# Kernel optimization log

Measured on AMD Instinct MI355X. Metric: run time of the kernel, lower is better.

Reference implementation:

```python
import jax, jax.numpy as jnp
import numpy as np


def setup_inputs() -> dict:
    key = jax.random.key(0)
    k1, k2, k3, k4, k5 = jax.random.split(key, 5)
    M, K, N, E = 16384, 2048, 5632, 8  # total_tokens, d_model, expert ffn dim, num_experts
    a = jax.random.normal(k1, (M, K), jnp.float32) * 0.1          # fp8-valued activations (simulated in f32)
    b = jax.random.normal(k2, (E, N, K), jnp.float32) * 0.05      # column-major expert weights [E, N, K]
    scale_a = jax.random.uniform(k3, (M, 1), jnp.float32, 0.5, 1.5)   # per-token dequant scale
    scale_b = jax.random.uniform(k4, (E, 1), jnp.float32, 0.5, 1.5)   # per-expert dequant scale
    cuts = jnp.sort(jax.random.randint(k5, (E - 1,), 0, M)).astype(jnp.int32)
    seg_indptr = jnp.concatenate([jnp.zeros(1, jnp.int32), cuts, jnp.full((1,), M, jnp.int32)])
    return {"a": a, "b": b, "scale_a": scale_a, "scale_b": scale_b,
            "seg_indptr": seg_indptr, "batch_size": E}


def reference(a, b, scale_a, scale_b, seg_indptr, batch_size):
    # Grouped GEMM: for expert e, rows seg_indptr[e]:seg_indptr[e+1] of `a` are
    # multiplied by b[e]^T (b is column-major [E, N, K]).
    M = a.shape[0]
    E = b.shape[0]
    group_sizes = jnp.diff(seg_indptr).astype(jnp.int32)           # [E]
    out = jax.lax.ragged_dot(a, jnp.swapaxes(b, 1, 2), group_sizes)  # [M, N]
    # fp8 w8a8 dequant: per-token scale_a, per-expert scale_b gathered per token
    eid = jnp.clip(jnp.searchsorted(seg_indptr, jnp.arange(M), side='right') - 1, 0, E - 1)
    return out * scale_a * scale_b[eid]
```

## Files before the change

kernel.cpp:

```cpp
#include <hip/hip_runtime.h>


#define BK 32
#define NKSTEP 64
#define KDIM 2048

typedef __attribute__((ext_vector_type(4))) float f32x4;
typedef __attribute__((ext_vector_type(4))) unsigned int u32x4;
using frag_ab = __attribute__((ext_vector_type(8))) short;
using frag_cd = __attribute__((ext_vector_type(4))) float;

__device__ __forceinline__ unsigned int pack_bf2(float x, float y) {
  unsigned int ux = __float_as_uint(x);
  unsigned int uy = __float_as_uint(y);
  ux += 0x7fffu + ((ux >> 16) & 1u);
  uy += 0x7fffu + ((uy >> 16) & 1u);
  return (ux >> 16) | (uy & 0xffff0000u);
}

__device__ __forceinline__ void gload_lds16(const void* g, void* lds) {
  __builtin_amdgcn_global_load_lds(
      (const __attribute__((address_space(1))) unsigned int*)g,
      (__attribute__((address_space(3))) unsigned int*)lds, 16, 0, 0);
}

__global__ __launch_bounds__(256)
void convert_kernel(const float* __restrict__ A, const float* __restrict__ B,
                    unsigned short* __restrict__ wa, unsigned short* __restrict__ wb) {
  constexpr long long NA = 16384LL * 2048;
  constexpr long long NB = 8LL * 5632 * 2048;
  constexpr long long NA8 = NA / 8;
  constexpr long long NTOT = (NA + NB) / 8;
  for (long long c = (long long)blockIdx.x * 256 + threadIdx.x; c < NTOT;
       c += (long long)gridDim.x * 256) {
    const float* src;
    unsigned short* dst;
    long long off;
    if (c < NA8) { src = A; dst = wa; off = c * 8; }
    else         { src = B; dst = wb; off = (c - NA8) * 8; }
    f32x4 v0 = *(const f32x4*)(src + off);
    f32x4 v1 = *(const f32x4*)(src + off + 4);
    u32x4 o;
    o[0] = pack_bf2(v0[0], v0[1]);
    o[1] = pack_bf2(v0[2], v0[3]);
    o[2] = pack_bf2(v1[0], v1[1]);
    o[3] = pack_bf2(v1[2], v1[3]);
    *(u32x4*)(dst + off) = o;
  }
}

__global__ __launch_bounds__(256, 3)
void ggemm_o(const unsigned short* __restrict__ A,
             const unsigned short* __restrict__ B,
             const float* __restrict__ sa,
             const float* __restrict__ sb,
             const int* __restrict__ seg,
             float* __restrict__ C) {
  constexpr int M = 16384, N = 5632, E = 8;
  constexpr int NTC = N / 128;
  const int nwg = (M / 128) * NTC;

  int bid = blockIdx.x;
  int sid = (bid & 7) * (nwg >> 3) + (bid >> 3);
  int mt = sid / NTC, nt = sid % NTC;
  int m0 = mt * 128, n0 = nt * 128;

  int tid = threadIdx.x, lane = tid & 63, w = tid >> 6;
  int wr = (w >> 1) * 64, wc = (w & 1) * 64;
  int l16 = lane & 15, lhi = lane >> 4;

  __shared__ unsigned short Asm[2][128 * 32];
  __shared__ unsigned short Bsm[2][128 * 32];

  int sr = lane >> 2;
  int scol = (((lane & 3) ^ (sr & 3)) * 8);
  const unsigned short* gA = A + (size_t)(m0 + w * 32 + sr) * KDIM + scol;

  int xA[4], xB[4];
#pragma unroll
  for (int i = 0; i < 4; ++i)
    xA[i] = (wr + i * 16 + l16) * 32 + ((lhi ^ (l16 & 3)) * 8);
#pragma unroll
  for (int j = 0; j < 4; ++j)
    xB[j] = (wc + j * 16 + l16) * 32 + ((lhi ^ (l16 & 3)) * 8);

  for (int e = 0; e < E; ++e) {
    int rlo = max(m0, seg[e]);
    int rhi = min(m0 + 128, seg[e + 1]);
    if (rlo >= rhi) continue;
    const unsigned short* gB =
        B + (size_t)e * N * KDIM + (size_t)(n0 + w * 32 + sr) * KDIM + scol;

    frag_cd acc[4][4];
#pragma unroll
    for (int i = 0; i < 4; ++i)
#pragma unroll
      for (int j = 0; j < 4; ++j) acc[i][j] = (frag_cd){0.f, 0.f, 0.f, 0.f};

    auto stage = [&](int b, int kt) {
#pragma unroll
      for (int i = 0; i < 2; ++i) {
        gload_lds16(gA + (size_t)i * 16 * KDIM + kt * BK,
                    &Asm[b][(w * 32 + i * 16) * 32]);
        gload_lds16(gB + (size_t)i * 16 * KDIM + kt * BK,
                    &Bsm[b][(w * 32 + i * 16) * 32]);
      }
    };
    auto compute = [&](int b) {
      frag_ab af[4], bf[4];
#pragma unroll
      for (int i = 0; i < 4; ++i) af[i] = *(const frag_ab*)(&Asm[b][xA[i]]);
#pragma unroll
      for (int j = 0; j < 4; ++j) bf[j] = *(const frag_ab*)(&Bsm[b][xB[j]]);
#pragma unroll
      for (int i = 0; i < 4; ++i)
#pragma unroll
        for (int j = 0; j < 4; ++j)
          acc[i][j] = __builtin_amdgcn_mfma_f32_16x16x32_bf16(
              af[i], bf[j], acc[i][j], 0, 0, 0);
    };

    stage(0, 0);
    __syncthreads();
    for (int kt = 0; kt < NKSTEP; ++kt) {
      if (kt + 1 < NKSTEP) stage((kt + 1) & 1, kt + 1);
      compute(kt & 1);
      __syncthreads();
    }

    float sbe = sb[e];
#pragma unroll
    for (int i = 0; i < 4; ++i) {
#pragma unroll
      for (int r = 0; r < 4; ++r) {
        int grow = m0 + wr + i * 16 + lhi * 4 + r;
        if (grow >= rlo && grow < rhi) {
          float s = sa[grow] * sbe;
          float* Crow = C + (size_t)grow * N + n0 + wc;
#pragma unroll
          for (int j = 0; j < 4; ++j)
            Crow[j * 16 + l16] = acc[i][j][r] * s;
        }
      }
    }
  }
}

extern "C" void kernel_launch(void* const* d_in, const int* in_sizes, int n_in,
                              void* d_out, int out_size, void* d_ws, size_t ws_size,
                              hipStream_t stream) {
  const float* a = (const float*)d_in[0];
  const float* b = (const float*)d_in[1];
  const float* sa = (const float*)d_in[2];
  const float* sb = (const float*)d_in[3];
  const int* seg = (const int*)d_in[4];
  float* out = (float*)d_out;

  constexpr size_t NA = 16384ULL * 2048;
  unsigned short* wa = (unsigned short*)d_ws;
  unsigned short* wb = wa + NA;

  hipLaunchKernelGGL(convert_kernel, dim3(2048), dim3(256), 0, stream, a, b, wa, wb);
  hipLaunchKernelGGL(ggemm_o, dim3(5632), dim3(256), 0, stream,
                     wa, wb, sa, sb, seg, out);
}
```

Measured before the change: 774.0 us.

## Double K-tile depth to 64 and remap workgroups into XCD-local super-tiles

The GEMM K tile grows from 32 to 64, with a new 8-way XOR swizzle for the wider LDS rows. This halves the number of barriers and stage/compute iterations and gives two MFMA k-substeps per sync. The block-to-tile mapping now keeps each XCD on a contiguous band of 16 M-tiles, walked in 8x11 super-tiles, to improve L2 reuse of A and B. LDS use doubles and the occupancy hint drops from 3 to 2 blocks per CU.

```diff
diff --git a/kernel.cpp b/kernel.cpp
--- a/kernel.cpp
+++ b/kernel.cpp
@@ -1,8 +1,8 @@
 #include <hip/hip_runtime.h>
 
 
-#define BK 32
-#define NKSTEP 64
+#define BK 64
+#define NKSTEP 32
 #define KDIM 2048
 
 typedef __attribute__((ext_vector_type(4))) float f32x4;
@@ -49,47 +49,51 @@
   }
 }
 
-__global__ __launch_bounds__(256, 3)
-void ggemm_o(const unsigned short* __restrict__ A,
+__global__ __launch_bounds__(256, 2)
+void ggemm_s(const unsigned short* __restrict__ A,
              const unsigned short* __restrict__ B,
              const float* __restrict__ sa,
              const float* __restrict__ sb,
              const int* __restrict__ seg,
              float* __restrict__ C) {
   constexpr int M = 16384, N = 5632, E = 8;
-  constexpr int NTC = N / 128;
-  const int nwg = (M / 128) * NTC;
 
   int bid = blockIdx.x;
-  int sid = (bid & 7) * (nwg >> 3) + (bid >> 3);
-  int mt = sid / NTC, nt = sid % NTC;
+  int xcd = bid & 7;
+  int r = bid >> 3;
+  int st = r / 88, p = r % 88;
+  int pm = p & 7, pn = p >> 3;
+  int smt = st >> 2, snt = st & 3;
+  int mt = xcd * 16 + smt * 8 + pm;
+  int nt = snt * 11 + pn;
   int m0 = mt * 128, n0 = nt * 128;
 
   int tid = threadIdx.x, lane = tid & 63, w = tid >> 6;
   int wr = (w >> 1) * 64, wc = (w & 1) * 64;
   int l16 = lane & 15, lhi = lane >> 4;
 
-  __shared__ unsigned short Asm[2][128 * 32];
-  __shared__ unsigned short Bsm[2][128 * 32];
+  __shared__ unsigned short Asm[2][128 * 64];
+  __shared__ unsigned short Bsm[2][128 * 64];
 
-  int sr = lane >> 2;
-  int scol = (((lane & 3) ^ (sr & 3)) * 8);
-  const unsigned short* gA = A + (size_t)(m0 + w * 32 + sr) * KDIM + scol;
+  int srow = lane >> 3;
+  int scol = ((lane & 7) ^ srow) * 8;
+  const unsigned short* gA = A + (size_t)(m0 + w * 32 + srow) * KDIM + scol;
 
-  int xA[4], xB[4];
+  int c7 = l16 & 7;
+  int x0 = (lhi ^ c7) * 8;
+  int x1 = ((4 | lhi) ^ c7) * 8;
+  int offA[4], offB[4];
 #pragma unroll
-  for (int i = 0; i < 4; ++i)
-    xA[i] = (wr + i * 16 + l16) * 32 + ((lhi ^ (l16 & 3)) * 8);
+  for (int i = 0; i < 4; ++i) offA[i] = (wr + i * 16 + l16) * 64;
 #pragma unroll
-  for (int j = 0; j < 4; ++j)
-    xB[j] = (wc + j * 16 + l16) * 32 + ((lhi ^ (l16 & 3)) * 8);
+  for (int j = 0; j < 4; ++j) offB[j] = (wc + j * 16 + l16) * 64;
 
   for (int e = 0; e < E; ++e) {
     int rlo = max(m0, seg[e]);
     int rhi = min(m0 + 128, seg[e + 1]);
     if (rlo >= rhi) continue;
     const unsigned short* gB =
-        B + (size_t)e * N * KDIM + (size_t)(n0 + w * 32 + sr) * KDIM + scol;
+        B + (size_t)e * N * KDIM + (size_t)(n0 + w * 32 + srow) * KDIM + scol;
 
     frag_cd acc[4][4];
 #pragma unroll
@@ -99,25 +103,31 @@
 
     auto stage = [&](int b, int kt) {
 #pragma unroll
-      for (int i = 0; i < 2; ++i) {
-        gload_lds16(gA + (size_t)i * 16 * KDIM + kt * BK,
-                    &Asm[b][(w * 32 + i * 16) * 32]);
-        gload_lds16(gB + (size_t)i * 16 * KDIM + kt * BK,
-                    &Bsm[b][(w * 32 + i * 16) * 32]);
+      for (int i = 0; i < 4; ++i) {
+        gload_lds16(gA + (size_t)i * 8 * KDIM + kt * BK,
+                    &Asm[b][(w * 32 + i * 8) * 64]);
+        gload_lds16(gB + (size_t)i * 8 * KDIM + kt * BK,
+                    &Bsm[b][(w * 32 + i * 8) * 64]);
       }
     };
     auto compute = [&](int b) {
-      frag_ab af[4], bf[4];
+      const unsigned short* pa = &Asm[b][0];
+      const unsigned short* pb = &Bsm[b][0];
 #pragma unroll
-      for (int i = 0; i < 4; ++i) af[i] = *(const frag_ab*)(&Asm[b][xA[i]]);
+      for (int ks = 0; ks < 2; ++ks) {
+        int x = ks ? x1 : x0;
+        frag_ab af[4], bf[4];
 #pragma unroll
-      for (int j = 0; j < 4; ++j) bf[j] = *(const frag_ab*)(&Bsm[b][xB[j]]);
+        for (int i = 0; i < 4; ++i) af[i] = *(const frag_ab*)(pa + offA[i] + x);
 #pragma unroll
-      for (int i = 0; i < 4; ++i)
+        for (int j = 0; j < 4; ++j) bf[j] = *(const frag_ab*)(pb + offB[j] + x);
 #pragma unroll
-        for (int j = 0; j < 4; ++j)
-          acc[i][j] = __builtin_amdgcn_mfma_f32_16x16x32_bf16(
-              af[i], bf[j], acc[i][j], 0, 0, 0);
+        for (int i = 0; i < 4; ++i)
+#pragma unroll
+          for (int j = 0; j < 4; ++j)
+            acc[i][j] = __builtin_amdgcn_mfma_f32_16x16x32_bf16(
+                af[i], bf[j], acc[i][j], 0, 0, 0);
+      }
     };
 
     stage(0, 0);
@@ -132,14 +142,14 @@
 #pragma unroll
     for (int i = 0; i < 4; ++i) {
 #pragma unroll
-      for (int r = 0; r < 4; ++r) {
-        int grow = m0 + wr + i * 16 + lhi * 4 + r;
+      for (int rr = 0; rr < 4; ++rr) {
+        int grow = m0 + wr + i * 16 + lhi * 4 + rr;
         if (grow >= rlo && grow < rhi) {
           float s = sa[grow] * sbe;
           float* Crow = C + (size_t)grow * N + n0 + wc;
 #pragma unroll
           for (int j = 0; j < 4; ++j)
-            Crow[j * 16 + l16] = acc[i][j][r] * s;
+            Crow[j * 16 + l16] = acc[i][j][rr] * s;
         }
       }
     }
@@ -161,6 +171,6 @@
   unsigned short* wb = wa + NA;
 
   hipLaunchKernelGGL(convert_kernel, dim3(2048), dim3(256), 0, stream, a, b, wa, wb);
-  hipLaunchKernelGGL(ggemm_o, dim3(5632), dim3(256), 0, stream,
+  hipLaunchKernelGGL(ggemm_s, dim3(5632), dim3(256), 0, stream,
                      wa, wb, sa, sb, seg, out);
 }
```

Result: slower. 930.1 us (+20.2%).
